# Kernel optimization log

Measured on AMD Instinct MI355X. Metric: run time of the kernel, lower is better.

## Reference

```python
import jax, jax.numpy as jnp
import numpy as np

EPS = 1e-8  # torch.nn.CosineSimilarity default eps


def setup_inputs() -> dict:
    key = jax.random.key(0)
    k1, k2, k3 = jax.random.split(key, 3)
    B, D = 4096, 768
    x = jax.random.normal(k1, (B, D), dtype=jnp.float32)
    fc_w = jax.random.normal(k2, (2, 1), dtype=jnp.float32) * (1.0)  # Linear(1,2) weight
    fc_b = jax.random.normal(k3, (2,), dtype=jnp.float32)
    return {"x": x, "fc_w": fc_w, "fc_b": fc_b}


def reference(x, fc_w, fc_b):
    # Pairwise cosine similarity via normalize-then-GEMM.
    # torch CosineSimilarity: dot(a,b) / (max(||a||, eps) * max(||b||, eps))
    norms = jnp.maximum(jnp.linalg.norm(x, axis=-1, keepdims=True), EPS)  # [B,1]
    xn = x / norms                                                        # [B,D]
    sim = jnp.einsum('id,jd->ij', xn, xn)                                 # [B,B]
    # fc: Linear(1,2) on sim.unsqueeze(-1): out[...,k] = sim * w[k,0] + b[k]
    out = sim[..., None] * fc_w[:, 0] + fc_b                              # [B,B,2]
    return out
```

## Files before the change

kernel.cpp:

```cpp
#include <hip/hip_runtime.h>
#include <hip/hip_bf16.h>

typedef int i32x4 __attribute__((ext_vector_type(4)));
typedef int i32x8 __attribute__((ext_vector_type(8)));
typedef float f32x4 __attribute__((ext_vector_type(4)));

#define KD 768
#define BDIM 4096
#define NSTRIP 16
#define E8M0_1_8TH 124
#define BLDS 24576

#define GLOAD_LDS16(gptr, lptr)                                             \
    __builtin_amdgcn_global_load_lds(                                       \
        (const __attribute__((address_space(1))) unsigned int*)(gptr),      \
        (__attribute__((address_space(3))) unsigned int*)(lptr), 16, 0, 0)

#define FBAR() asm volatile("s_barrier" ::: "memory")
#define SCHED_FENCE() __builtin_amdgcn_sched_barrier(0)

__device__ inline unsigned char f32_to_e4m3(float f) {
    int p = __builtin_amdgcn_cvt_pk_fp8_f32(f, f, 0, false);
    return (unsigned char)(p & 0xFF);
}

__global__ __launch_bounds__(256) void normalize_rows_fp8(
    const float* __restrict__ x, unsigned char* __restrict__ xn)
{
    const int row = blockIdx.x;
    const int t = threadIdx.x;
    const float* xr = x + (long)row * KD;

    float v[3];
    float ss = 0.f;
#pragma unroll
    for (int i = 0; i < 3; ++i) {
        v[i] = xr[t + 256 * i];
        ss += v[i] * v[i];
    }
#pragma unroll
    for (int off = 32; off > 0; off >>= 1) ss += __shfl_down(ss, off);
    __shared__ float wss[4];
    const int lane = t & 63, wv = t >> 6;
    if (lane == 0) wss[wv] = ss;
    __syncthreads();
    const float tot = wss[0] + wss[1] + wss[2] + wss[3];
    const float inv = 8.0f / fmaxf(sqrtf(tot), 1e-8f);
#pragma unroll
    for (int i = 0; i < 3; ++i)
        xn[(long)row * KD + t + 256 * i] = f32_to_e4m3(v[i] * inv);
}

__global__ __launch_bounds__(512, 4) void sim_gemm_stream(
    const unsigned char* __restrict__ Xn,
    const float* __restrict__ fcw, const float* __restrict__ fcb,
    float* __restrict__ out)
{
    __shared__ __align__(16) unsigned char Bb[2][BLDS];

    const int tid = threadIdx.x;
    const int wv  = tid >> 6;
    const int ln  = tid & 63;
    const int wm  = wv >> 1;
    const int wn  = wv & 1;
    const int fr  = ln & 15;
    const int q   = ln >> 4;

    const int jc = blockIdx.x;
    const int bi = blockIdx.y;
    const long Arow0 = (long)bi * 64;
    const long Bcol0 = (long)jc * 512;

    int scol[3], skoff[3];
#pragma unroll
    for (int i = 0; i < 3; ++i) {
        const int d = i * 8192 + tid * 16;
        scol[i]  = (d >> 6) & 31;
        skoff[i] = ((d >> 12) << 7) + (((d >> 4) & 3) << 5) + (((d >> 11) & 1) << 4);
    }

#define ISSUE_B(s) do {                                                      \
        _Pragma("unroll")                                                    \
        for (int i_ = 0; i_ < 3; ++i_) {                                     \
            const unsigned char* g_ = Xn                                     \
                + (Bcol0 + (s) * 32 + scol[i_]) * (long)KD + skoff[i_];      \
            unsigned char* l_ = &Bb[(s) & 1][0] + i_ * 8192 + wv * 1024;     \
            GLOAD_LDS16(g_, l_);                                             \
        }                                                                    \
    } while (0)

    i32x8 aF[6];
    {
        const unsigned char* pa = Xn + (Arow0 + wm * 16 + fr) * (long)KD + q * 32;
#pragma unroll
        for (int kk = 0; kk < 6; ++kk) {
            i32x4 lo = *(const i32x4*)(pa + kk * 128);
            i32x4 hi = *(const i32x4*)(pa + kk * 128 + 16);
            aF[kk] = __builtin_shufflevector(lo, hi, 0, 1, 2, 3, 4, 5, 6, 7);
        }
    }

    const float w0 = fcw[0], w1 = fcw[1];
    const float c0 = fcb[0], c1 = fcb[1];

    ISSUE_B(0);
    asm volatile("s_waitcnt vmcnt(0)" ::: "memory");
    FBAR();

    const int colbase = (int)Bcol0 + wn * 16 + fr;
    const long rowb   = Arow0 + wm * 16 + q * 4;

    for (int s = 0; s < NSTRIP; ++s) {
        const int bb = s & 1;

        if (s + 1 < NSTRIP) ISSUE_B(s + 1);
        SCHED_FENCE();

        f32x4 acc = {};
#pragma unroll
        for (int kk = 0; kk < 6; ++kk) {
            const int bo = kk * 4096 + (wn * 16 + fr) * 64 + q * 16;
            i32x4 lo = *(const i32x4*)&Bb[bb][bo];
            i32x4 hi = *(const i32x4*)&Bb[bb][bo + 2048];
            i32x8 bv = __builtin_shufflevector(lo, hi, 0, 1, 2, 3, 4, 5, 6, 7);
            __builtin_amdgcn_s_setprio(1);
            acc = __builtin_amdgcn_mfma_scale_f32_16x16x128_f8f6f4(
                aF[kk], bv, acc, 0, 0, 0, E8M0_1_8TH, 0, E8M0_1_8TH);
            __builtin_amdgcn_s_setprio(0);
        }

        const int col = colbase + s * 32;
#pragma unroll
        for (int rr = 0; rr < 4; ++rr) {
            const long row = rowb + rr;
            const float sv = acc[rr];
            *(float2*)&out[(row * BDIM + col) * 2] =
                make_float2(fmaf(sv, w0, c0), fmaf(sv, w1, c1));
        }

        if (s + 1 < NSTRIP) {
            asm volatile("s_waitcnt vmcnt(4)" ::: "memory");
            FBAR();
        }
    }

#undef ISSUE_B
}

extern "C" void kernel_launch(void* const* d_in, const int* in_sizes, int n_in,
                              void* d_out, int out_size, void* d_ws, size_t ws_size,
                              hipStream_t stream) {
    const float* x   = (const float*)d_in[0];
    const float* fcw = (const float*)d_in[1];
    const float* fcb = (const float*)d_in[2];
    float* out = (float*)d_out;

    unsigned char* xn = (unsigned char*)d_ws;

    normalize_rows_fp8<<<BDIM, 256, 0, stream>>>(x, xn);

    dim3 grid(8, 64);
    sim_gemm_stream<<<grid, 512, 0, stream>>>(xn, fcw, fcb, out);
}
```

Before: 40.00 us.

## Replace LDS-staged strip GEMM with row-panel kernel loading B directly from global

The GEMM kernel is restructured so that each block computes a 16-row panel across all 4096 columns, with each wave covering 512 columns. B fragments are read straight from global memory into registers instead of being staged through double-buffered LDS with barriers. All 32 accumulators are held before the output is written. This removes the LDS traffic and synchronisation, but each wave now reloads B from global/L2 and register pressure rises, so occupancy drops and a lot of output sits in registers before it is stored.

```diff
diff --git a/kernel.cpp b/kernel.cpp
--- a/kernel.cpp
+++ b/kernel.cpp
@@ -7,17 +7,7 @@
 
 #define KD 768
 #define BDIM 4096
-#define NSTRIP 16
 #define E8M0_1_8TH 124
-#define BLDS 24576
-
-#define GLOAD_LDS16(gptr, lptr)                                             \
-    __builtin_amdgcn_global_load_lds(                                       \
-        (const __attribute__((address_space(1))) unsigned int*)(gptr),      \
-        (__attribute__((address_space(3))) unsigned int*)(lptr), 16, 0, 0)
-
-#define FBAR() asm volatile("s_barrier" ::: "memory")
-#define SCHED_FENCE() __builtin_amdgcn_sched_barrier(0)
 
 __device__ inline unsigned char f32_to_e4m3(float f) {
     int p = __builtin_amdgcn_cvt_pk_fp8_f32(f, f, 0, false);
@@ -51,47 +41,24 @@
         xn[(long)row * KD + t + 256 * i] = f32_to_e4m3(v[i] * inv);
 }
 
-__global__ __launch_bounds__(512, 4) void sim_gemm_stream(
+__global__ __launch_bounds__(512, 2) void sim_gemm_rowpanel(
     const unsigned char* __restrict__ Xn,
     const float* __restrict__ fcw, const float* __restrict__ fcb,
     float* __restrict__ out)
 {
-    __shared__ __align__(16) unsigned char Bb[2][BLDS];
-
     const int tid = threadIdx.x;
     const int wv  = tid >> 6;
     const int ln  = tid & 63;
-    const int wm  = wv >> 1;
-    const int wn  = wv & 1;
     const int fr  = ln & 15;
     const int q   = ln >> 4;
 
-    const int jc = blockIdx.x;
-    const int bi = blockIdx.y;
-    const long Arow0 = (long)bi * 64;
-    const long Bcol0 = (long)jc * 512;
-
-    int scol[3], skoff[3];
-#pragma unroll
-    for (int i = 0; i < 3; ++i) {
-        const int d = i * 8192 + tid * 16;
-        scol[i]  = (d >> 6) & 31;
-        skoff[i] = ((d >> 12) << 7) + (((d >> 4) & 3) << 5) + (((d >> 11) & 1) << 4);
-    }
-
-#define ISSUE_B(s) do {                                                      \
-        _Pragma("unroll")                                                    \
-        for (int i_ = 0; i_ < 3; ++i_) {                                     \
-            const unsigned char* g_ = Xn                                     \
-                + (Bcol0 + (s) * 32 + scol[i_]) * (long)KD + skoff[i_];      \
-            unsigned char* l_ = &Bb[(s) & 1][0] + i_ * 8192 + wv * 1024;     \
-            GLOAD_LDS16(g_, l_);                                             \
-        }                                                                    \
-    } while (0)
+    const int bi = blockIdx.x;
+    const long Arow0 = (long)bi * 16;
+    const int  wcol0 = wv * 512;
 
     i32x8 aF[6];
     {
-        const unsigned char* pa = Xn + (Arow0 + wm * 16 + fr) * (long)KD + q * 32;
+        const unsigned char* pa = Xn + (Arow0 + fr) * (long)KD + q * 32;
 #pragma unroll
         for (int kk = 0; kk < 6; ++kk) {
             i32x4 lo = *(const i32x4*)(pa + kk * 128);
@@ -100,51 +67,36 @@
         }
     }
 
+    f32x4 acc[32];
+    const unsigned char* pb0 = Xn + ((long)wcol0 + fr) * KD + q * 32;
+#pragma unroll
+    for (int cf = 0; cf < 32; ++cf) {
+        const unsigned char* pb = pb0 + (long)cf * 16 * KD;
+        f32x4 a = {};
+#pragma unroll
+        for (int kk = 0; kk < 6; ++kk) {
+            i32x4 lo = *(const i32x4*)(pb + kk * 128);
+            i32x4 hi = *(const i32x4*)(pb + kk * 128 + 16);
+            i32x8 bv = __builtin_shufflevector(lo, hi, 0, 1, 2, 3, 4, 5, 6, 7);
+            a = __builtin_amdgcn_mfma_scale_f32_16x16x128_f8f6f4(
+                aF[kk], bv, a, 0, 0, 0, E8M0_1_8TH, 0, E8M0_1_8TH);
+        }
+        acc[cf] = a;
+    }
+
     const float w0 = fcw[0], w1 = fcw[1];
     const float c0 = fcb[0], c1 = fcb[1];
-
-    ISSUE_B(0);
-    asm volatile("s_waitcnt vmcnt(0)" ::: "memory");
-    FBAR();
-
-    const int colbase = (int)Bcol0 + wn * 16 + fr;
-    const long rowb   = Arow0 + wm * 16 + q * 4;
-
-    for (int s = 0; s < NSTRIP; ++s) {
-        const int bb = s & 1;
-
-        if (s + 1 < NSTRIP) ISSUE_B(s + 1);
-        SCHED_FENCE();
-
-        f32x4 acc = {};
 #pragma unroll
-        for (int kk = 0; kk < 6; ++kk) {
-            const int bo = kk * 4096 + (wn * 16 + fr) * 64 + q * 16;
-            i32x4 lo = *(const i32x4*)&Bb[bb][bo];
-            i32x4 hi = *(const i32x4*)&Bb[bb][bo + 2048];
-            i32x8 bv = __builtin_shufflevector(lo, hi, 0, 1, 2, 3, 4, 5, 6, 7);
-            __builtin_amdgcn_s_setprio(1);
-            acc = __builtin_amdgcn_mfma_scale_f32_16x16x128_f8f6f4(
-                aF[kk], bv, acc, 0, 0, 0, E8M0_1_8TH, 0, E8M0_1_8TH);
-            __builtin_amdgcn_s_setprio(0);
-        }
-
-        const int col = colbase + s * 32;
+    for (int rr = 0; rr < 4; ++rr) {
+        const long row = Arow0 + q * 4 + rr;
+        float* po = out + (row * BDIM + wcol0 + fr) * 2;
 #pragma unroll
-        for (int rr = 0; rr < 4; ++rr) {
-            const long row = rowb + rr;
-            const float sv = acc[rr];
-            *(float2*)&out[(row * BDIM + col) * 2] =
+        for (int cf = 0; cf < 32; ++cf) {
+            const float sv = acc[cf][rr];
+            *(float2*)(po + cf * 32) =
                 make_float2(fmaf(sv, w0, c0), fmaf(sv, w1, c1));
         }
-
-        if (s + 1 < NSTRIP) {
-            asm volatile("s_waitcnt vmcnt(4)" ::: "memory");
-            FBAR();
-        }
     }
-
-#undef ISSUE_B
 }
 
 extern "C" void kernel_launch(void* const* d_in, const int* in_sizes, int n_in,
@@ -159,6 +111,5 @@
 
     normalize_rows_fp8<<<BDIM, 256, 0, stream>>>(x, xn);
 
-    dim3 grid(8, 64);
-    sim_gemm_stream<<<grid, 512, 0, stream>>>(xn, fcw, fcb, out);
+    sim_gemm_rowpanel<<<BDIM / 16, 512, 0, stream>>>(xn, fcw, fcb, out);
 }
```

Measured after the change: 118.5 us. 2.96x slower.
